# Kernel tuning notes

Hardware: AMD Instinct MI355X
Metric: run time of the kernel (lower is better)

The kernel has to match this reference:

```python
import jax, jax.numpy as jnp
import numpy as np

EPS = 1e-8
K_KNN = 20

def vn_lin(W, x):
    # W: [Cout, Cin], x: [B, Cin, 3, ...] -> [B, Cout, 3, ...]
    return jnp.einsum('oi,bi...->bo...', W, x)

def vn_relu(Wd, x):
    # VNLeakyReLU with negative_slope=0, share_nonlinearity=False
    d = jnp.einsum('oi,bi...->bo...', Wd, x)
    dot = jnp.sum(x * d, axis=2, keepdims=True)   # sum over 3-vector axis
    dsq = jnp.sum(d * d, axis=2, keepdims=True) + EPS
    return jnp.where(dot >= 0, x, x - (dot / dsq) * d)

def graph_feature_cross(p, k):
    # p: [B, N, 3] -> feat: [B, 3, 3, N, k]
    xx = jnp.sum(p * p, axis=-1)                       # [B,N]
    inner = jnp.einsum('bnd,bmd->bnm', p, p)           # [B,N,N]
    neg_dist = 2.0 * inner - xx[:, :, None] - xx[:, None, :]
    idx = jax.lax.top_k(neg_dist, k)[1]                # [B,N,k] nearest neighbors
    nbrs = jax.vmap(lambda pb, ib: pb[ib])(p, idx)     # [B,N,k,3]
    xr = jnp.broadcast_to(p[:, :, None, :], nbrs.shape)
    cross = jnp.cross(nbrs, xr)                        # [B,N,k,3]
    feat = jnp.stack([nbrs - xr, xr, cross], axis=3)   # [B,N,k,3(ch),3(vec)]
    return jnp.transpose(feat, (0, 3, 4, 1, 2))        # [B,3,3,N,k]

def setup_inputs() -> dict:
    key = jax.random.key(0)
    ks = jax.random.split(key, 9)
    B, N = 4, 2048
    H = 128           # hidden_dim // 3
    C_IN = 2 * H      # 256
    CC = 128          # c_dim // 3
    s_in = 1.0 / np.sqrt(C_IN)
    s_h = 1.0 / np.sqrt(H)
    return {
        'p': jax.random.normal(ks[0], (B, N, 3), dtype=jnp.float32),
        'fc_pos_W': jax.random.normal(ks[1], (C_IN, 3), dtype=jnp.float32) / np.sqrt(3.0),
        'blk_d0': jax.random.normal(ks[2], (5, C_IN, C_IN), dtype=jnp.float32) * s_in,
        'blk_W0': jax.random.normal(ks[3], (5, H, C_IN), dtype=jnp.float32) * s_in,
        'blk_d1': jax.random.normal(ks[4], (5, H, H), dtype=jnp.float32) * s_h,
        'blk_W1': jax.random.normal(ks[5], (5, H, H), dtype=jnp.float32) * s_h,
        'blk_Ws': jax.random.normal(ks[6], (5, H, C_IN), dtype=jnp.float32) * s_in,
        'fc_c_W': jax.random.normal(ks[7], (CC, H), dtype=jnp.float32) * s_h,
        'act_d': jax.random.normal(ks[8], (H, H), dtype=jnp.float32) * s_h,
    }

def reference(p, fc_pos_W, blk_d0, blk_W0, blk_d1, blk_W1, blk_Ws, fc_c_W, act_d):
    feat = graph_feature_cross(p, K_KNN)          # [B,3,3,N,k]
    x = vn_lin(fc_pos_W, feat)                    # [B,256,3,N,k]
    net = jnp.mean(x, axis=-1)                    # mean_pool over k -> [B,256,3,N]

    def block(i, x):
        h = vn_lin(blk_W0[i], vn_relu(blk_d0[i], x))
        dx = vn_lin(blk_W1[i], vn_relu(blk_d1[i], h))
        return vn_lin(blk_Ws[i], x) + dx          # shortcut (size_in != size_out)

    net = block(0, net)                           # [B,128,3,N]
    for i in range(1, 5):
        pooled = jnp.broadcast_to(jnp.mean(net, axis=3, keepdims=True), net.shape)
        net = block(i, jnp.concatenate([net, pooled], axis=1))
    net = jnp.mean(net, axis=3)                   # [B,128,3]
    c = vn_lin(fc_c_W, vn_relu(act_d, net))       # [B,128,3]
    return c.reshape(c.shape[0], -1)              # [B,384]
```

## Files before the change

kernel.cpp:

```cpp
#include <hip/hip_runtime.h>
#include <math.h>

#define N_PTS 2048
#define K_NN  20
#define K_D   10
#define WTOT  819200

typedef unsigned short u16;
typedef unsigned int   u32;
typedef _Float16 f16;
using half8   = __attribute__((ext_vector_type(8))) _Float16;
using floatx4 = __attribute__((ext_vector_type(4))) float;

__device__ __forceinline__ void split2h(float v, f16& h, f16& l) {
    h = (f16)v;
    l = (f16)((v - (float)h) * 1024.0f);
}

__device__ __forceinline__ float neg_dist(float4 q2, float4 c) {
    return fmaf(q2.x, c.x, fmaf(q2.y, c.y, fmaf(q2.z, c.z, -q2.w))) - c.w;
}

__global__ __launch_bounds__(256) void prep_kernel(
    const float* __restrict__ pts, float* __restrict__ m_out,
    const float* __restrict__ bd0, const float* __restrict__ bW0,
    const float* __restrict__ bd1, const float* __restrict__ bW1,
    const float* __restrict__ bWs, u16* __restrict__ Wswz,
    float* __restrict__ nm_acc)
{
    __shared__ float4 sp[N_PTS];
    if (blockIdx.x >= 1024) {
        int i = (blockIdx.x - 1024) * 256 + threadIdx.x;
        if (i >= WTOT) return;
        if (i < 7680) nm_acc[i] = 0.f;
        float v; int base, K, local;
        if (i < 327680)      { int rel = i;          base = (rel/65536)*65536;            local = rel%65536; K = 256; v = bd0[rel]; }
        else if (i < 491520) { int rel = i - 327680; base = 327680 + (rel/32768)*32768;   local = rel%32768; K = 256; v = bW0[rel]; }
        else if (i < 573440) { int rel = i - 491520; base = 491520 + (rel/16384)*16384;   local = rel%16384; K = 128; v = bd1[rel]; }
        else if (i < 655360) { int rel = i - 573440; base = 573440 + (rel/16384)*16384;   local = rel%16384; K = 128; v = bW1[rel]; }
        else                 { int rel = i - 655360; base = 655360 + (rel/32768)*32768;   local = rel%32768; K = 256; v = bWs[rel]; }
        int m = local / K, k = local % K;
        int NKF = K >> 5;
        int mf = m >> 4, r = m & 15;
        int kf = k >> 5, q = (k >> 3) & 3, ii = k & 7;
        int lane = q*16 + r;
        int dst = base + ((mf*NKF + kf)*64 + lane)*8 + ii;
        f16 h, l; split2h(v, h, l);
        f16* W = (f16*)Wswz;
        W[dst] = h; W[WTOT + dst] = l;
        return;
    }

    const int b     = blockIdx.x >> 8;
    const int qbase = (blockIdx.x & 255) << 3;
    const int ql    = threadIdx.x >> 5;
    const int sl    = threadIdx.x & 31;
    const float* pb = pts + (size_t)b * N_PTS * 3;
    for (int i = threadIdx.x; i < N_PTS; i += 256) {
        float x = pb[i*3+0], y = pb[i*3+1], z = pb[i*3+2];
        sp[i] = make_float4(x, y, z, x*x + y*y + z*z);
    }
    __syncthreads();

    const int n = qbase + ql;
    const float4 q = sp[n];
    const float4 q2 = make_float4(2.f*q.x, 2.f*q.y, 2.f*q.z, q.w);

    float t[K_D];
#pragma unroll
    for (int s = 0; s < K_D; ++s) t[s] = -INFINITY;

    for (int j = 0; j < N_PTS/32; ++j) {
        float4 c = sp[j*32 + sl];
        float v = neg_dist(q2, c);
#pragma unroll
        for (int s = 0; s < K_D; ++s) {
            float nx = (s < K_D-1) ? t[s+1] : INFINITY;
            t[s] = fminf(fmaxf(t[s], v), nx);
        }
    }

    float head = t[K_D-1];
    float T = -INFINITY;
#pragma unroll 1
    for (int e = 0; e < K_NN; ++e) {
        float v = head; int w = sl;
#pragma unroll
        for (int off = 1; off < 32; off <<= 1) {
            float vo = __shfl_xor(v, off);
            int   wo = __shfl_xor(w, off);
            bool take = (vo > v) || (vo == v && wo < w);
            v = take ? vo : v;
            w = take ? wo : w;
        }
        T = v;
        if (w == sl) {
#pragma unroll
            for (int s = K_D-1; s > 0; --s) t[s] = t[s-1];
            t[0] = -INFINITY;
            head = t[K_D-1];
        }
    }

    float sx = 0.f, sy = 0.f, sz = 0.f;
    for (int j = 0; j < N_PTS/32; ++j) {
        float4 c = sp[j*32 + sl];
        float v = neg_dist(q2, c);
        if (v >= T) { sx += c.x; sy += c.y; sz += c.z; }
    }
#pragma unroll
    for (int off = 1; off < 32; off <<= 1) {
        sx += __shfl_xor(sx, off);
        sy += __shfl_xor(sy, off);
        sz += __shfl_xor(sz, off);
    }
    if (sl == 0) {
        const float inv = 1.0f / (float)K_NN;
        const int pt = b * N_PTS + n;
        m_out[pt*3+0] = sx * inv;
        m_out[pt*3+1] = sy * inv;
        m_out[pt*3+2] = sz * inv;
    }
}

template<int MF, int JF>
__device__ __forceinline__ void run_gemm_hi(
    const f16* __restrict__ Whi, size_t aoff,
    int NK, const f16* Blds, int bstride, int lane,
    floatx4 (&acc)[MF][JF])
{
    const int l15 = lane & 15;
    const int lq8 = (lane >> 4) * 8;
    half8 Aa[MF], Ab[MF];

    auto loada = [&](half8 (&dst)[MF], int kf) {
#pragma unroll
        for (int fm = 0; fm < MF; ++fm)
            dst[fm] = *(const half8*)(Whi + aoff + (size_t)(fm*NK + kf)*512 + (size_t)lane*8);
    };
    auto step = [&](half8 (&af)[MF], int kf) {
        half8 bq[JF];
#pragma unroll
        for (int fj = 0; fj < JF; ++fj)
            bq[fj] = *(const half8*)&Blds[(fj*16 + l15)*bstride + kf*32 + lq8];
#pragma unroll
        for (int fm = 0; fm < MF; ++fm)
#pragma unroll
            for (int fj = 0; fj < JF; ++fj)
                acc[fm][fj] = __builtin_amdgcn_mfma_f32_16x16x32_f16(af[fm], bq[fj], acc[fm][fj], 0, 0, 0);
    };

    loada(Aa, 0);
#pragma unroll 1
    for (int kf = 0; kf < NK; kf += 2) {
        loada(Ab, kf + 1);
        step(Aa, kf);
        if (kf + 2 < NK) loada(Aa, kf + 2);
        step(Ab, kf + 1);
    }
}

template<int MF, int JF>
__device__ __forceinline__ void run_gemm_split(
    const f16* __restrict__ Whi, const f16* __restrict__ Wlo, size_t aoff,
    int NK, const f16* Blds, int bstride, int lane,
    floatx4 (&acc)[MF][JF], floatx4 (&accL)[MF][JF])
{
    const int l15 = lane & 15;
    const int lq8 = (lane >> 4) * 8;
    half8 Aa[2*MF], Ab[2*MF];

    auto loada = [&](half8 (&dst)[2*MF], int kf) {
#pragma unroll
        for (int fm = 0; fm < MF; ++fm) {
            size_t fo = aoff + (size_t)(fm*NK + kf)*512 + (size_t)lane*8;
            dst[fm*2+0] = *(const half8*)(Whi + fo);
            dst[fm*2+1] = *(const half8*)(Wlo + fo);
        }
    };
    auto step = [&](half8 (&af)[2*MF], int kf) {
        half8 bq[JF];
#pragma unroll
        for (int fj = 0; fj < JF; ++fj)
            bq[fj] = *(const half8*)&Blds[(fj*16 + l15)*bstride + kf*32 + lq8];
#pragma unroll
        for (int fm = 0; fm < MF; ++fm)
#pragma unroll
            for (int fj = 0; fj < JF; ++fj) {
                acc[fm][fj]  = __builtin_amdgcn_mfma_f32_16x16x32_f16(af[fm*2+0], bq[fj], acc[fm][fj], 0, 0, 0);
                accL[fm][fj] = __builtin_amdgcn_mfma_f32_16x16x32_f16(af[fm*2+1], bq[fj], accL[fm][fj], 0, 0, 0);
            }
    };

    loada(Aa, 0);
#pragma unroll 1
    for (int kf = 0; kf < NK; kf += 2) {
        loada(Ab, kf + 1);
        step(Aa, kf);
        if (kf + 2 < NK) loada(Aa, kf + 2);
        step(Ab, kf + 1);
    }
}

__device__ __forceinline__ uint2 pack_res(floatx4 a, floatx4 aL) {
    u16 hh[4];
#pragma unroll
    for (int r = 0; r < 4; ++r) {
        f16 hv = (f16)(a[r] + aL[r] * (1.0f/1024.0f));
        hh[r] = *(u16*)&hv;
    }
    uint2 pv;
    pv.x = (u32)hh[0] | ((u32)hh[1] << 16);
    pv.y = (u32)hh[2] | ((u32)hh[3] << 16);
    return pv;
}

__device__ __forceinline__ uint2 pack_hi(floatx4 a) {
    u16 hh[4];
#pragma unroll
    for (int r = 0; r < 4; ++r) {
        f16 hv = (f16)a[r];
        hh[r] = *(u16*)&hv;
    }
    uint2 pv;
    pv.x = (u32)hh[0] | ((u32)hh[1] << 16);
    pv.y = (u32)hh[2] | ((u32)hh[3] << 16);
    return pv;
}

__global__ __launch_bounds__(256, 3) void resblk_kernel(
    const u16* __restrict__ Wswz,
    int offD0, int offW0, int offD1, int offW1, int offWs,
    const f16* __restrict__ netIn, const float* __restrict__ nm_prev,
    const float* __restrict__ pts, const float* __restrict__ m_buf,
    const float* __restrict__ fcW,
    f16* __restrict__ netOut, float* __restrict__ nm_out, int blk0,
    int skip_store)
{
    __shared__ struct {
        f16 X[48*264];
        union { f16 d[48*264]; float C[48*132]; } Y;
    } s;

    const int tid  = threadIdx.x;
    const int jb   = blockIdx.x * 48;
    const int bB   = blockIdx.x >> 7;
    const int lane = tid & 63;
    const int wv   = tid >> 6;
    const f16* Whi = (const f16*)Wswz;
    const f16* Wlo = Whi + WTOT;

    if (blk0) {
        float* Hf = (float*)s.Y.C;
        const int ptbase = blockIdx.x * 16;
        for (int i = tid; i < 768; i += 256) Hf[i] = fcW[i];
        if (tid < 96) Hf[768 + tid] = (tid < 48) ? pts[ptbase*3 + tid]
                                                 : m_buf[ptbase*3 + tid - 48];
        __syncthreads();
#pragma unroll 1
        for (int it = 0; it < 6; ++it) {
            int idx = tid + 256*it;
            int r = idx >> 5;
            int cg = idx & 31;
            int l = r / 3, v = r - l*3;
            float pv0[3] = {Hf[768+l*3], Hf[768+l*3+1], Hf[768+l*3+2]};
            float mv0[3] = {Hf[816+l*3], Hf[816+l*3+1], Hf[816+l*3+2]};
            int v1 = (v==2) ? 0 : v+1;
            int v2 = (v==0) ? 2 : v-1;
            float av = mv0[v] - pv0[v];
            float bv = pv0[v];
            float cv = mv0[v1]*pv0[v2] - mv0[v2]*pv0[v1];
            half8 o;
#pragma unroll
            for (int k = 0; k < 8; ++k) {
                int ch = cg*8 + k;
                o[k] = (f16)(Hf[ch*3+0]*av + Hf[ch*3+1]*bv + Hf[ch*3+2]*cv);
            }
            *(half8*)&s.X[r*264 + cg*8] = o;
        }
    } else {
#pragma unroll 1
        for (int it = 0; it < 6; ++it) {
            int idx = tid + 256*it;
            int r = idx >> 5;
            int cg = idx & 31;
            if (cg < 16) {
                uint4 vv = *(const uint4*)(netIn + (size_t)(jb + r)*128 + cg*8);
                *(uint4*)&s.X[r*264 + cg*8] = vv;
            } else {
                int v = r % 3;
                const float* np = nm_prev + (bB*3+v)*128 + (cg-16)*8;
                half8 o;
#pragma unroll
                for (int k = 0; k < 8; ++k) o[k] = (f16)(np[k] * (1.0f/2048.0f));
                *(half8*)&s.X[r*264 + cg*8] = o;
            }
        }
    }
    __syncthreads();

    floatx4 acc4[2][3], accL4[2][3];
#pragma unroll
    for (int a = 0; a < 2; ++a)
#pragma unroll
        for (int b = 0; b < 3; ++b) { acc4[a][b] = (floatx4){0,0,0,0}; accL4[a][b] = (floatx4){0,0,0,0}; }

    {
        floatx4 acc[4][3];
#pragma unroll
        for (int a = 0; a < 4; ++a)
#pragma unroll
            for (int b = 0; b < 3; ++b) acc[a][b] = (floatx4){0,0,0,0};
        run_gemm_hi<4,3>(Whi, (size_t)offD0 + (size_t)wv*16384, 8, s.X, 264, lane, acc);
#pragma unroll
        for (int fm = 0; fm < 4; ++fm)
#pragma unroll
            for (int fj = 0; fj < 3; ++fj) {
                int mloc = wv*64 + fm*16 + (lane>>4)*4;
                int jl   = fj*16 + (lane & 15);
                *(uint2*)&s.Y.d[jl*264 + mloc] = pack_hi(acc[fm][fj]);
            }
    }
    __syncthreads();

    run_gemm_split<2,3>(Whi, Wlo, (size_t)offWs + (size_t)wv*8192, 8, s.X, 264, lane, acc4, accL4);

#pragma unroll 1
    for (int it = 0; it < 2; ++it) {
        int idx = tid + 256*it;
        int l = idx >> 5, cg = idx & 31;
        half8 xa = *(const half8*)&s.X[(l*3+0)*264 + cg*8];
        half8 xb = *(const half8*)&s.X[(l*3+1)*264 + cg*8];
        half8 xc = *(const half8*)&s.X[(l*3+2)*264 + cg*8];
        half8 da = *(const half8*)&s.Y.d[(l*3+0)*264 + cg*8];
        half8 db = *(const half8*)&s.Y.d[(l*3+1)*264 + cg*8];
        half8 dc = *(const half8*)&s.Y.d[(l*3+2)*264 + cg*8];
        half8 ya, yb, yc;
#pragma unroll
        for (int k = 0; k < 8; ++k) {
            float x0 = (float)xa[k], x1 = (float)xb[k], x2 = (float)xc[k];
            float d0 = (float)da[k], d1 = (float)db[k], d2 = (float)dc[k];
            float dot = x0*d0 + x1*d1 + x2*d2;
            float y0, y1, y2;
            if (dot >= 0.f) { y0 = x0; y1 = x1; y2 = x2; }
            else {
                float dsq = d0*d0 + d1*d1 + d2*d2 + 1e-8f;
                float sc = dot / dsq;
                y0 = x0 - sc*d0; y1 = x1 - sc*d1; y2 = x2 - sc*d2;
            }
            ya[k] = (f16)y0; yb[k] = (f16)y1; yc[k] = (f16)y2;
        }
        *(half8*)&s.Y.d[(l*3+0)*264 + cg*8] = ya;
        *(half8*)&s.Y.d[(l*3+1)*264 + cg*8] = yb;
        *(half8*)&s.Y.d[(l*3+2)*264 + cg*8] = yc;
    }
    __syncthreads();

    {
        floatx4 acc[2][3], accL[2][3];
#pragma unroll
        for (int a = 0; a < 2; ++a)
#pragma unroll
            for (int b = 0; b < 3; ++b) { acc[a][b] = (floatx4){0,0,0,0}; accL[a][b] = (floatx4){0,0,0,0}; }
        run_gemm_split<2,3>(Whi, Wlo, (size_t)offW0 + (size_t)wv*8192, 8, s.Y.d, 264, lane, acc, accL);
#pragma unroll
        for (int fm = 0; fm < 2; ++fm)
#pragma unroll
            for (int fj = 0; fj < 3; ++fj) {
                int mloc = wv*32 + fm*16 + (lane>>4)*4;
                int jl   = fj*16 + (lane & 15);
                *(uint2*)&s.X[jl*136 + mloc] = pack_res(acc[fm][fj], accL[fm][fj]);
            }
    }
    __syncthreads();

    {
        floatx4 acc[2][3];
#pragma unroll
        for (int a = 0; a < 2; ++a)
#pragma unroll
            for (int b = 0; b < 3; ++b) acc[a][b] = (floatx4){0,0,0,0};
        run_gemm_hi<2,3>(Whi, (size_t)offD1 + (size_t)wv*4096, 4, s.X, 136, lane, acc);
#pragma unroll
        for (int fm = 0; fm < 2; ++fm)
#pragma unroll
            for (int fj = 0; fj < 3; ++fj) {
                int mloc = wv*32 + fm*16 + (lane>>4)*4;
                int jl   = fj*16 + (lane & 15);
                *(uint2*)&s.Y.d[jl*136 + mloc] = pack_hi(acc[fm][fj]);
            }
    }
    __syncthreads();

    {
        int l = tid >> 4, cg = tid & 15;
        half8 xa = *(const half8*)&s.X[(l*3+0)*136 + cg*8];
        half8 xb = *(const half8*)&s.X[(l*3+1)*136 + cg*8];
        half8 xc = *(const half8*)&s.X[(l*3+2)*136 + cg*8];
        half8 da = *(const half8*)&s.Y.d[(l*3+0)*136 + cg*8];
        half8 db = *(const half8*)&s.Y.d[(l*3+1)*136 + cg*8];
        half8 dc = *(const half8*)&s.Y.d[(l*3+2)*136 + cg*8];
        half8 ya, yb, yc;
#pragma unroll
        for (int k = 0; k < 8; ++k) {
            float x0 = (float)xa[k], x1 = (float)xb[k], x2 = (float)xc[k];
            float d0 = (float)da[k], d1 = (float)db[k], d2 = (float)dc[k];
            float dot = x0*d0 + x1*d1 + x2*d2;
            float y0, y1, y2;
            if (dot >= 0.f) { y0 = x0; y1 = x1; y2 = x2; }
            else {
                float dsq = d0*d0 + d1*d1 + d2*d2 + 1e-8f;
                float sc = dot / dsq;
                y0 = x0 - sc*d0; y1 = x1 - sc*d1; y2 = x2 - sc*d2;
            }
            ya[k] = (f16)y0; yb[k] = (f16)y1; yc[k] = (f16)y2;
        }
        __syncthreads();
        *(half8*)&s.X[(l*3+0)*136 + cg*8] = ya;
        *(half8*)&s.X[(l*3+1)*136 + cg*8] = yb;
        *(half8*)&s.X[(l*3+2)*136 + cg*8] = yc;
    }
    __syncthreads();

    run_gemm_split<2,3>(Whi, Wlo, (size_t)offW1 + (size_t)wv*4096, 4, s.X, 136, lane, acc4, accL4);

#pragma unroll
    for (int fm = 0; fm < 2; ++fm)
#pragma unroll
        for (int fj = 0; fj < 3; ++fj) {
            int mloc = wv*32 + fm*16 + (lane>>4)*4;
            int jl   = fj*16 + (lane & 15);
            floatx4 res;
#pragma unroll
            for (int r = 0; r < 4; ++r) res[r] = acc4[fm][fj][r] + accL4[fm][fj][r] * (1.0f/1024.0f);
            if (!skip_store) {
                u16 hh[4];
#pragma unroll
                for (int r = 0; r < 4; ++r) { f16 hv = (f16)res[r]; hh[r] = *(u16*)&hv; }
                uint2 pv;
                pv.x = (u32)hh[0] | ((u32)hh[1] << 16);
                pv.y = (u32)hh[2] | ((u32)hh[3] << 16);
                *(uint2*)(netOut + (size_t)(jb + jl)*128 + mloc) = pv;
            }
            *(floatx4*)&s.Y.C[jl*132 + mloc] = res;
        }
    __syncthreads();

#pragma unroll 1
    for (int idx = tid; idx < 384; idx += 256) {
        int v = idx >> 7, ch = idx & 127;
        float sum = 0.f;
#pragma unroll 1
        for (int pt = 0; pt < 16; ++pt) sum += s.Y.C[(pt*3+v)*132 + ch];
        atomicAdd(nm_out + (bB*3+v)*128 + ch, sum);
    }
}

__global__ __launch_bounds__(128) void final_kernel(const float* __restrict__ nm_sum,
                                                    const float* __restrict__ act_d,
                                                    const float* __restrict__ fc_c,
                                                    float* __restrict__ out)
{
    const int b = blockIdx.x;
    const int c = threadIdx.x;
    __shared__ float xs[128][3];
    __shared__ float ys[128][3];
    xs[c][0] = nm_sum[(b*3+0)*128 + c] * (1.0f/2048.0f);
    xs[c][1] = nm_sum[(b*3+1)*128 + c] * (1.0f/2048.0f);
    xs[c][2] = nm_sum[(b*3+2)*128 + c] * (1.0f/2048.0f);
    __syncthreads();
    float d0 = 0.f, d1 = 0.f, d2 = 0.f;
    for (int i = 0; i < 128; ++i) {
        float w = act_d[c*128 + i];
        d0 = fmaf(w, xs[i][0], d0);
        d1 = fmaf(w, xs[i][1], d1);
        d2 = fmaf(w, xs[i][2], d2);
    }
    float x0 = xs[c][0], x1 = xs[c][1], x2 = xs[c][2];
    float dot = x0*d0 + x1*d1 + x2*d2;
    float y0, y1, y2;
    if (dot >= 0.f) { y0 = x0; y1 = x1; y2 = x2; }
    else {
        float dsq = d0*d0 + d1*d1 + d2*d2 + 1e-8f;
        float sc = dot / dsq;
        y0 = x0 - sc*d0; y1 = x1 - sc*d1; y2 = x2 - sc*d2;
    }
    ys[c][0] = y0; ys[c][1] = y1; ys[c][2] = y2;
    __syncthreads();
    float o0 = 0.f, o1 = 0.f, o2 = 0.f;
    for (int i = 0; i < 128; ++i) {
        float w = fc_c[c*128 + i];
        o0 = fmaf(w, ys[i][0], o0);
        o1 = fmaf(w, ys[i][1], o1);
        o2 = fmaf(w, ys[i][2], o2);
    }
    out[b*384 + c*3 + 0] = o0;
    out[b*384 + c*3 + 1] = o1;
    out[b*384 + c*3 + 2] = o2;
}

extern "C" void kernel_launch(void* const* d_in, const int* in_sizes, int n_in,
                              void* d_out, int out_size, void* d_ws, size_t ws_size,
                              hipStream_t stream)
{
    const float* p      = (const float*)d_in[0];
    const float* fc_pos = (const float*)d_in[1];
    const float* bd0    = (const float*)d_in[2];
    const float* bW0    = (const float*)d_in[3];
    const float* bd1    = (const float*)d_in[4];
    const float* bW1    = (const float*)d_in[5];
    const float* bWs    = (const float*)d_in[6];
    const float* fc_c   = (const float*)d_in[7];
    const float* act_d  = (const float*)d_in[8];
    float* out = (float*)d_out;

    char* w = (char*)d_ws;
    float* m_buf  = (float*)w;  w += 98304;
    float* nm_acc = (float*)w;  w += 5*1536*4;
    u16*   Wswz   = (u16*)w;    w += (size_t)2*WTOT*2;
    f16*   netA   = (f16*)w;    w += (size_t)24576*128*2;
    f16*   netB   = (f16*)w;    w += (size_t)24576*128*2;

    prep_kernel<<<dim3(1024 + 3200), dim3(256), 0, stream>>>(
        p, m_buf, bd0, bW0, bd1, bW1, bWs, Wswz, nm_acc);

    f16* nIn = netA;
    f16* nOut = netB;
    for (int blk = 0; blk < 5; ++blk) {
        const int offD0 = blk*65536;
        const int offW0 = 327680 + blk*32768;
        const int offD1 = 491520 + blk*16384;
        const int offW1 = 573440 + blk*16384;
        const int offWs = 655360 + blk*32768;
        const float* nmp = (blk == 0) ? nullptr : (nm_acc + (blk-1)*1536);
        resblk_kernel<<<dim3(512), dim3(256), 0, stream>>>(
            Wswz, offD0, offW0, offD1, offW1, offWs,
            (blk == 0) ? netA : nIn, nmp, p, m_buf, fc_pos,
            nOut, nm_acc + blk*1536, (blk == 0) ? 1 : 0,
            (blk == 4) ? 1 : 0);
        f16* tmp = nIn; nIn = nOut; nOut = tmp;
    }

    final_kernel<<<dim3(4), dim3(128), 0, stream>>>(nm_acc + 4*1536, act_d, fc_c, out);

    (void)in_sizes; (void)n_in; (void)out_size; (void)ws_size;
}
```

Measured before the change: 241.2 us.

## Fuse five residual blocks and final head into one persistent kernel with grid barrier

Replaces the five resblk launches and the final kernel with a single persistent kernel. Blocks loop over the residual stages, keep each block's point features resident in shared memory, and synchronize the global pooled means with an atomic-counter grid barrier. This removes launch overhead and the global fp16 round trip of the intermediate net tensor. It relies on all 512 blocks being co-resident (3 per CU is assumed), which risks deadlock otherwise, and adds barrier spin latency.

```diff
diff --git a/kernel.cpp b/kernel.cpp
--- a/kernel.cpp
+++ b/kernel.cpp
@@ -26,13 +26,14 @@
     const float* __restrict__ bd0, const float* __restrict__ bW0,
     const float* __restrict__ bd1, const float* __restrict__ bW1,
     const float* __restrict__ bWs, u16* __restrict__ Wswz,
-    float* __restrict__ nm_acc)
+    float* __restrict__ nm_acc, int* __restrict__ bar)
 {
     __shared__ float4 sp[N_PTS];
     if (blockIdx.x >= 1024) {
         int i = (blockIdx.x - 1024) * 256 + threadIdx.x;
         if (i >= WTOT) return;
         if (i < 7680) nm_acc[i] = 0.f;
+        if (i == 0) bar[0] = 0;
         float v; int base, K, local;
         if (i < 327680)      { int rel = i;          base = (rel/65536)*65536;            local = rel%65536; K = 256; v = bd0[rel]; }
         else if (i < 491520) { int rel = i - 327680; base = 327680 + (rel/32768)*32768;   local = rel%32768; K = 256; v = bW0[rel]; }
@@ -228,14 +229,25 @@
     return pv;
 }
 
-__global__ __launch_bounds__(256, 3) void resblk_kernel(
+__device__ __forceinline__ void grid_barrier(int* cnt, int target, int wait) {
+    __threadfence();
+    __syncthreads();
+    if (threadIdx.x == 0) {
+        atomicAdd(cnt, 1);
+        if (wait) {
+            while (atomicAdd(cnt, 0) < target) __builtin_amdgcn_s_sleep(16);
+        }
+    }
+    __syncthreads();
+}
+
+__global__ __launch_bounds__(256, 3) void mega_kernel(
     const u16* __restrict__ Wswz,
-    int offD0, int offW0, int offD1, int offW1, int offWs,
-    const f16* __restrict__ netIn, const float* __restrict__ nm_prev,
+    float* __restrict__ nm_acc, int* __restrict__ bar,
     const float* __restrict__ pts, const float* __restrict__ m_buf,
     const float* __restrict__ fcW,
-    f16* __restrict__ netOut, float* __restrict__ nm_out, int blk0,
-    int skip_store)
+    const float* __restrict__ act_d, const float* __restrict__ fc_c,
+    float* __restrict__ out)
 {
     __shared__ struct {
         f16 X[48*264];
@@ -243,103 +255,243 @@
     } s;
 
     const int tid  = threadIdx.x;
-    const int jb   = blockIdx.x * 48;
     const int bB   = blockIdx.x >> 7;
     const int lane = tid & 63;
     const int wv   = tid >> 6;
     const f16* Whi = (const f16*)Wswz;
     const f16* Wlo = Whi + WTOT;
 
-    if (blk0) {
-        float* Hf = (float*)s.Y.C;
-        const int ptbase = blockIdx.x * 16;
-        for (int i = tid; i < 768; i += 256) Hf[i] = fcW[i];
-        if (tid < 96) Hf[768 + tid] = (tid < 48) ? pts[ptbase*3 + tid]
-                                                 : m_buf[ptbase*3 + tid - 48];
-        __syncthreads();
-#pragma unroll 1
-        for (int it = 0; it < 6; ++it) {
+#pragma unroll 1
+    for (int blk = 0; blk < 5; ++blk) {
+        const int offD0 = blk*65536;
+        const int offW0 = 327680 + blk*32768;
+        const int offD1 = 491520 + blk*16384;
+        const int offW1 = 573440 + blk*16384;
+        const int offWs = 655360 + blk*32768;
+        float* nm_out = nm_acc + blk*1536;
+
+        if (blk == 0) {
+            float* Hf = (float*)s.Y.C;
+            const int ptbase = blockIdx.x * 16;
+            for (int i = tid; i < 768; i += 256) Hf[i] = fcW[i];
+            if (tid < 96) Hf[768 + tid] = (tid < 48) ? pts[ptbase*3 + tid]
+                                                     : m_buf[ptbase*3 + tid - 48];
+            __syncthreads();
+#pragma unroll 1
+            for (int it = 0; it < 6; ++it) {
+                int idx = tid + 256*it;
+                int r = idx >> 5;
+                int cgp = idx & 31;
+                int l = r / 3, v = r - l*3;
+                float pv0[3] = {Hf[768+l*3], Hf[768+l*3+1], Hf[768+l*3+2]};
+                float mv0[3] = {Hf[816+l*3], Hf[816+l*3+1], Hf[816+l*3+2]};
+                int v1 = (v==2) ? 0 : v+1;
+                int v2 = (v==0) ? 2 : v-1;
+                float av = mv0[v] - pv0[v];
+                float bv = pv0[v];
+                float cv = mv0[v1]*pv0[v2] - mv0[v2]*pv0[v1];
+                half8 o;
+#pragma unroll
+                for (int k = 0; k < 8; ++k) {
+                    int ch = cgp*8 + k;
+                    o[k] = (f16)(Hf[ch*3+0]*av + Hf[ch*3+1]*bv + Hf[ch*3+2]*cv);
+                }
+                *(half8*)&s.X[r*264 + cgp*8] = o;
+            }
+        } else {
+            f16* nmv = &s.Y.d[0];
+#pragma unroll 1
+            for (int idx = tid; idx < 384; idx += 256) {
+                int v = idx >> 7, ch = idx & 127;
+                float sv = atomicAdd(&nm_acc[(blk-1)*1536 + (bB*3+v)*128 + ch], 0.0f);
+                nmv[v*128 + ch] = (f16)(sv * (1.0f/2048.0f));
+            }
+            __syncthreads();
+#pragma unroll 1
+            for (int it = 0; it < 3; ++it) {
+                int idx = tid + 256*it;
+                int r = idx >> 4;
+                int cgp = idx & 15;
+                int v = r % 3;
+                *(uint4*)&s.X[r*264 + 128 + cgp*8] = *(const uint4*)&nmv[v*128 + cgp*8];
+            }
+        }
+        __syncthreads();
+
+        floatx4 acc4[2][3], accL4[2][3];
+#pragma unroll
+        for (int a = 0; a < 2; ++a)
+#pragma unroll
+            for (int b = 0; b < 3; ++b) { acc4[a][b] = (floatx4){0,0,0,0}; accL4[a][b] = (floatx4){0,0,0,0}; }
+
+        {
+            floatx4 acc[4][3];
+#pragma unroll
+            for (int a = 0; a < 4; ++a)
+#pragma unroll
+                for (int b = 0; b < 3; ++b) acc[a][b] = (floatx4){0,0,0,0};
+            run_gemm_hi<4,3>(Whi, (size_t)offD0 + (size_t)wv*16384, 8, s.X, 264, lane, acc);
+#pragma unroll
+            for (int fm = 0; fm < 4; ++fm)
+#pragma unroll
+                for (int fj = 0; fj < 3; ++fj) {
+                    int mloc = wv*64 + fm*16 + (lane>>4)*4;
+                    int jl   = fj*16 + (lane & 15);
+                    *(uint2*)&s.Y.d[jl*264 + mloc] = pack_hi(acc[fm][fj]);
+                }
+        }
+        __syncthreads();
+
+        run_gemm_split<2,3>(Whi, Wlo, (size_t)offWs + (size_t)wv*8192, 8, s.X, 264, lane, acc4, accL4);
+
+#pragma unroll 1
+        for (int it = 0; it < 2; ++it) {
             int idx = tid + 256*it;
-            int r = idx >> 5;
-            int cg = idx & 31;
-            int l = r / 3, v = r - l*3;
-            float pv0[3] = {Hf[768+l*3], Hf[768+l*3+1], Hf[768+l*3+2]};
-            float mv0[3] = {Hf[816+l*3], Hf[816+l*3+1], Hf[816+l*3+2]};
-            int v1 = (v==2) ? 0 : v+1;
-            int v2 = (v==0) ? 2 : v-1;
-            float av = mv0[v] - pv0[v];
-            float bv = pv0[v];
-            float cv = mv0[v1]*pv0[v2] - mv0[v2]*pv0[v1];
-            half8 o;
+            int l = idx >> 5, cgp = idx & 31;
+            half8 xa = *(const half8*)&s.X[(l*3+0)*264 + cgp*8];
+            half8 xb = *(const half8*)&s.X[(l*3+1)*264 + cgp*8];
+            half8 xc = *(const half8*)&s.X[(l*3+2)*264 + cgp*8];
+            half8 da = *(const half8*)&s.Y.d[(l*3+0)*264 + cgp*8];
+            half8 db = *(const half8*)&s.Y.d[(l*3+1)*264 + cgp*8];
+            half8 dc = *(const half8*)&s.Y.d[(l*3+2)*264 + cgp*8];
+            half8 ya, yb, yc;
 #pragma unroll
             for (int k = 0; k < 8; ++k) {
-                int ch = cg*8 + k;
-                o[k] = (f16)(Hf[ch*3+0]*av + Hf[ch*3+1]*bv + Hf[ch*3+2]*cv);
-            }
-            *(half8*)&s.X[r*264 + cg*8] = o;
-        }
-    } else {
-#pragma unroll 1
-        for (int it = 0; it < 6; ++it) {
-            int idx = tid + 256*it;
-            int r = idx >> 5;
-            int cg = idx & 31;
-            if (cg < 16) {
-                uint4 vv = *(const uint4*)(netIn + (size_t)(jb + r)*128 + cg*8);
-                *(uint4*)&s.X[r*264 + cg*8] = vv;
-            } else {
-                int v = r % 3;
-                const float* np = nm_prev + (bB*3+v)*128 + (cg-16)*8;
-                half8 o;
-#pragma unroll
-                for (int k = 0; k < 8; ++k) o[k] = (f16)(np[k] * (1.0f/2048.0f));
-                *(half8*)&s.X[r*264 + cg*8] = o;
-            }
-        }
-    }
-    __syncthreads();
-
-    floatx4 acc4[2][3], accL4[2][3];
-#pragma unroll
-    for (int a = 0; a < 2; ++a)
-#pragma unroll
-        for (int b = 0; b < 3; ++b) { acc4[a][b] = (floatx4){0,0,0,0}; accL4[a][b] = (floatx4){0,0,0,0}; }
-
-    {
-        floatx4 acc[4][3];
-#pragma unroll
-        for (int a = 0; a < 4; ++a)
-#pragma unroll
-            for (int b = 0; b < 3; ++b) acc[a][b] = (floatx4){0,0,0,0};
-        run_gemm_hi<4,3>(Whi, (size_t)offD0 + (size_t)wv*16384, 8, s.X, 264, lane, acc);
-#pragma unroll
-        for (int fm = 0; fm < 4; ++fm)
+                float x0 = (float)xa[k], x1 = (float)xb[k], x2 = (float)xc[k];
+                float d0 = (float)da[k], d1 = (float)db[k], d2 = (float)dc[k];
+                float dot = x0*d0 + x1*d1 + x2*d2;
+                float y0, y1, y2;
+                if (dot >= 0.f) { y0 = x0; y1 = x1; y2 = x2; }
+                else {
+                    float dsq = d0*d0 + d1*d1 + d2*d2 + 1e-8f;
+                    float sc = dot / dsq;
+                    y0 = x0 - sc*d0; y1 = x1 - sc*d1; y2 = x2 - sc*d2;
+                }
+                ya[k] = (f16)y0; yb[k] = (f16)y1; yc[k] = (f16)y2;
+            }
+            *(half8*)&s.Y.d[(l*3+0)*264 + cgp*8] = ya;
+            *(half8*)&s.Y.d[(l*3+1)*264 + cgp*8] = yb;
+            *(half8*)&s.Y.d[(l*3+2)*264 + cgp*8] = yc;
+        }
+        __syncthreads();
+
+        {
+            floatx4 acc[2][3], accL[2][3];
+#pragma unroll
+            for (int a = 0; a < 2; ++a)
+#pragma unroll
+                for (int b = 0; b < 3; ++b) { acc[a][b] = (floatx4){0,0,0,0}; accL[a][b] = (floatx4){0,0,0,0}; }
+            run_gemm_split<2,3>(Whi, Wlo, (size_t)offW0 + (size_t)wv*8192, 8, s.Y.d, 264, lane, acc, accL);
+#pragma unroll
+            for (int fm = 0; fm < 2; ++fm)
+#pragma unroll
+                for (int fj = 0; fj < 3; ++fj) {
+                    int mloc = wv*32 + fm*16 + (lane>>4)*4;
+                    int jl   = fj*16 + (lane & 15);
+                    *(uint2*)&s.X[jl*136 + mloc] = pack_res(acc[fm][fj], accL[fm][fj]);
+                }
+        }
+        __syncthreads();
+
+        {
+            floatx4 acc[2][3];
+#pragma unroll
+            for (int a = 0; a < 2; ++a)
+#pragma unroll
+                for (int b = 0; b < 3; ++b) acc[a][b] = (floatx4){0,0,0,0};
+            run_gemm_hi<2,3>(Whi, (size_t)offD1 + (size_t)wv*4096, 4, s.X, 136, lane, acc);
+#pragma unroll
+            for (int fm = 0; fm < 2; ++fm)
+#pragma unroll
+                for (int fj = 0; fj < 3; ++fj) {
+                    int mloc = wv*32 + fm*16 + (lane>>4)*4;
+                    int jl   = fj*16 + (lane & 15);
+                    *(uint2*)&s.Y.d[jl*136 + mloc] = pack_hi(acc[fm][fj]);
+                }
+        }
+        __syncthreads();
+
+        {
+            int l = tid >> 4, cgp = tid & 15;
+            half8 xa = *(const half8*)&s.X[(l*3+0)*136 + cgp*8];
+            half8 xb = *(const half8*)&s.X[(l*3+1)*136 + cgp*8];
+            half8 xc = *(const half8*)&s.X[(l*3+2)*136 + cgp*8];
+            half8 da = *(const half8*)&s.Y.d[(l*3+0)*136 + cgp*8];
+            half8 db = *(const half8*)&s.Y.d[(l*3+1)*136 + cgp*8];
+            half8 dc = *(const half8*)&s.Y.d[(l*3+2)*136 + cgp*8];
+            half8 ya, yb, yc;
+#pragma unroll
+            for (int k = 0; k < 8; ++k) {
+                float x0 = (float)xa[k], x1 = (float)xb[k], x2 = (float)xc[k];
+                float d0 = (float)da[k], d1 = (float)db[k], d2 = (float)dc[k];
+                float dot = x0*d0 + x1*d1 + x2*d2;
+                float y0, y1, y2;
+                if (dot >= 0.f) { y0 = x0; y1 = x1; y2 = x2; }
+                else {
+                    float dsq = d0*d0 + d1*d1 + d2*d2 + 1e-8f;
+                    float sc = dot / dsq;
+                    y0 = x0 - sc*d0; y1 = x1 - sc*d1; y2 = x2 - sc*d2;
+                }
+                ya[k] = (f16)y0; yb[k] = (f16)y1; yc[k] = (f16)y2;
+            }
+            __syncthreads();
+            *(half8*)&s.X[(l*3+0)*136 + cgp*8] = ya;
+            *(half8*)&s.X[(l*3+1)*136 + cgp*8] = yb;
+            *(half8*)&s.X[(l*3+2)*136 + cgp*8] = yc;
+        }
+        __syncthreads();
+
+        run_gemm_split<2,3>(Whi, Wlo, (size_t)offW1 + (size_t)wv*4096, 4, s.X, 136, lane, acc4, accL4);
+        __syncthreads();
+
+#pragma unroll
+        for (int fm = 0; fm < 2; ++fm)
 #pragma unroll
             for (int fj = 0; fj < 3; ++fj) {
-                int mloc = wv*64 + fm*16 + (lane>>4)*4;
+                int mloc = wv*32 + fm*16 + (lane>>4)*4;
                 int jl   = fj*16 + (lane & 15);
-                *(uint2*)&s.Y.d[jl*264 + mloc] = pack_hi(acc[fm][fj]);
-            }
-    }
-    __syncthreads();
-
-    run_gemm_split<2,3>(Whi, Wlo, (size_t)offWs + (size_t)wv*8192, 8, s.X, 264, lane, acc4, accL4);
-
-#pragma unroll 1
-    for (int it = 0; it < 2; ++it) {
-        int idx = tid + 256*it;
-        int l = idx >> 5, cg = idx & 31;
-        half8 xa = *(const half8*)&s.X[(l*3+0)*264 + cg*8];
-        half8 xb = *(const half8*)&s.X[(l*3+1)*264 + cg*8];
-        half8 xc = *(const half8*)&s.X[(l*3+2)*264 + cg*8];
-        half8 da = *(const half8*)&s.Y.d[(l*3+0)*264 + cg*8];
-        half8 db = *(const half8*)&s.Y.d[(l*3+1)*264 + cg*8];
-        half8 dc = *(const half8*)&s.Y.d[(l*3+2)*264 + cg*8];
-        half8 ya, yb, yc;
-#pragma unroll
-        for (int k = 0; k < 8; ++k) {
-            float x0 = (float)xa[k], x1 = (float)xb[k], x2 = (float)xc[k];
-            float d0 = (float)da[k], d1 = (float)db[k], d2 = (float)dc[k];
+                floatx4 res;
+#pragma unroll
+                for (int r = 0; r < 4; ++r) res[r] = acc4[fm][fj][r] + accL4[fm][fj][r] * (1.0f/1024.0f);
+                *(uint2*)&s.X[jl*264 + mloc] = pack_res(acc4[fm][fj], accL4[fm][fj]);
+                *(floatx4*)&s.Y.C[jl*132 + mloc] = res;
+            }
+        __syncthreads();
+
+#pragma unroll 1
+        for (int idx = tid; idx < 384; idx += 256) {
+            int v = idx >> 7, ch = idx & 127;
+            float sum = 0.f;
+#pragma unroll 1
+            for (int pt = 0; pt < 16; ++pt) sum += s.Y.C[(pt*3+v)*132 + ch];
+            atomicAdd(nm_out + (bB*3+v)*128 + ch, sum);
+        }
+
+        int need_wait = (blk < 4) || (blockIdx.x < 4);
+        grid_barrier(bar, 512*(blk+1), need_wait);
+    }
+
+    if (blockIdx.x < 4) {
+        const int b = blockIdx.x;
+        float* xs = s.Y.C;
+        float* ys = s.Y.C + 384;
+        float* nm4 = nm_acc + 4*1536;
+        const int c = tid & 127;
+        if (tid < 128) {
+            xs[c*3+0] = atomicAdd(&nm4[(b*3+0)*128 + c], 0.0f) * (1.0f/2048.0f);
+            xs[c*3+1] = atomicAdd(&nm4[(b*3+1)*128 + c], 0.0f) * (1.0f/2048.0f);
+            xs[c*3+2] = atomicAdd(&nm4[(b*3+2)*128 + c], 0.0f) * (1.0f/2048.0f);
+        }
+        __syncthreads();
+        if (tid < 128) {
+            float d0 = 0.f, d1 = 0.f, d2 = 0.f;
+            for (int i = 0; i < 128; ++i) {
+                float w = act_d[c*128 + i];
+                d0 = fmaf(w, xs[i*3+0], d0);
+                d1 = fmaf(w, xs[i*3+1], d1);
+                d2 = fmaf(w, xs[i*3+2], d2);
+            }
+            float x0 = xs[c*3+0], x1 = xs[c*3+1], x2 = xs[c*3+2];
             float dot = x0*d0 + x1*d1 + x2*d2;
             float y0, y1, y2;
             if (dot >= 0.f) { y0 = x0; y1 = x1; y2 = x2; }
@@ -348,155 +500,22 @@
                 float sc = dot / dsq;
                 y0 = x0 - sc*d0; y1 = x1 - sc*d1; y2 = x2 - sc*d2;
             }
-            ya[k] = (f16)y0; yb[k] = (f16)y1; yc[k] = (f16)y2;
-        }
-        *(half8*)&s.Y.d[(l*3+0)*264 + cg*8] = ya;
-        *(half8*)&s.Y.d[(l*3+1)*264 + cg*8] = yb;
-        *(half8*)&s.Y.d[(l*3+2)*264 + cg*8] = yc;
-    }
-    __syncthreads();
-
-    {
-        floatx4 acc[2][3], accL[2][3];
-#pragma unroll
-        for (int a = 0; a < 2; ++a)
-#pragma unroll
-            for (int b = 0; b < 3; ++b) { acc[a][b] = (floatx4){0,0,0,0}; accL[a][b] = (floatx4){0,0,0,0}; }
-        run_gemm_split<2,3>(Whi, Wlo, (size_t)offW0 + (size_t)wv*8192, 8, s.Y.d, 264, lane, acc, accL);
-#pragma unroll
-        for (int fm = 0; fm < 2; ++fm)
-#pragma unroll
-            for (int fj = 0; fj < 3; ++fj) {
-                int mloc = wv*32 + fm*16 + (lane>>4)*4;
-                int jl   = fj*16 + (lane & 15);
-                *(uint2*)&s.X[jl*136 + mloc] = pack_res(acc[fm][fj], accL[fm][fj]);
-            }
-    }
-    __syncthreads();
-
-    {
-        floatx4 acc[2][3];
-#pragma unroll
-        for (int a = 0; a < 2; ++a)
-#pragma unroll
-            for (int b = 0; b < 3; ++b) acc[a][b] = (floatx4){0,0,0,0};
-        run_gemm_hi<2,3>(Whi, (size_t)offD1 + (size_t)wv*4096, 4, s.X, 136, lane, acc);
-#pragma unroll
-        for (int fm = 0; fm < 2; ++fm)
-#pragma unroll
-            for (int fj = 0; fj < 3; ++fj) {
-                int mloc = wv*32 + fm*16 + (lane>>4)*4;
-                int jl   = fj*16 + (lane & 15);
-                *(uint2*)&s.Y.d[jl*136 + mloc] = pack_hi(acc[fm][fj]);
-            }
-    }
-    __syncthreads();
-
-    {
-        int l = tid >> 4, cg = tid & 15;
-        half8 xa = *(const half8*)&s.X[(l*3+0)*136 + cg*8];
-        half8 xb = *(const half8*)&s.X[(l*3+1)*136 + cg*8];
-        half8 xc = *(const half8*)&s.X[(l*3+2)*136 + cg*8];
-        half8 da = *(const half8*)&s.Y.d[(l*3+0)*136 + cg*8];
-        half8 db = *(const half8*)&s.Y.d[(l*3+1)*136 + cg*8];
-        half8 dc = *(const half8*)&s.Y.d[(l*3+2)*136 + cg*8];
-        half8 ya, yb, yc;
-#pragma unroll
-        for (int k = 0; k < 8; ++k) {
-            float x0 = (float)xa[k], x1 = (float)xb[k], x2 = (float)xc[k];
-            float d0 = (float)da[k], d1 = (float)db[k], d2 = (float)dc[k];
-            float dot = x0*d0 + x1*d1 + x2*d2;
-            float y0, y1, y2;
-            if (dot >= 0.f) { y0 = x0; y1 = x1; y2 = x2; }
-            else {
-                float dsq = d0*d0 + d1*d1 + d2*d2 + 1e-8f;
-                float sc = dot / dsq;
-                y0 = x0 - sc*d0; y1 = x1 - sc*d1; y2 = x2 - sc*d2;
-            }
-            ya[k] = (f16)y0; yb[k] = (f16)y1; yc[k] = (f16)y2;
-        }
-        __syncthreads();
-        *(half8*)&s.X[(l*3+0)*136 + cg*8] = ya;
-        *(half8*)&s.X[(l*3+1)*136 + cg*8] = yb;
-        *(half8*)&s.X[(l*3+2)*136 + cg*8] = yc;
-    }
-    __syncthreads();
-
-    run_gemm_split<2,3>(Whi, Wlo, (size_t)offW1 + (size_t)wv*4096, 4, s.X, 136, lane, acc4, accL4);
-
-#pragma unroll
-    for (int fm = 0; fm < 2; ++fm)
-#pragma unroll
-        for (int fj = 0; fj < 3; ++fj) {
-            int mloc = wv*32 + fm*16 + (lane>>4)*4;
-            int jl   = fj*16 + (lane & 15);
-            floatx4 res;
-#pragma unroll
-            for (int r = 0; r < 4; ++r) res[r] = acc4[fm][fj][r] + accL4[fm][fj][r] * (1.0f/1024.0f);
-            if (!skip_store) {
-                u16 hh[4];
-#pragma unroll
-                for (int r = 0; r < 4; ++r) { f16 hv = (f16)res[r]; hh[r] = *(u16*)&hv; }
-                uint2 pv;
-                pv.x = (u32)hh[0] | ((u32)hh[1] << 16);
-                pv.y = (u32)hh[2] | ((u32)hh[3] << 16);
-                *(uint2*)(netOut + (size_t)(jb + jl)*128 + mloc) = pv;
-            }
-            *(floatx4*)&s.Y.C[jl*132 + mloc] = res;
-        }
-    __syncthreads();
-
-#pragma unroll 1
-    for (int idx = tid; idx < 384; idx += 256) {
-        int v = idx >> 7, ch = idx & 127;
-        float sum = 0.f;
-#pragma unroll 1
-        for (int pt = 0; pt < 16; ++pt) sum += s.Y.C[(pt*3+v)*132 + ch];
-        atomicAdd(nm_out + (bB*3+v)*128 + ch, sum);
-    }
-}
-
-__global__ __launch_bounds__(128) void final_kernel(const float* __restrict__ nm_sum,
-                                                    const float* __restrict__ act_d,
-                                                    const float* __restrict__ fc_c,
-                                                    float* __restrict__ out)
-{
-    const int b = blockIdx.x;
-    const int c = threadIdx.x;
-    __shared__ float xs[128][3];
-    __shared__ float ys[128][3];
-    xs[c][0] = nm_sum[(b*3+0)*128 + c] * (1.0f/2048.0f);
-    xs[c][1] = nm_sum[(b*3+1)*128 + c] * (1.0f/2048.0f);
-    xs[c][2] = nm_sum[(b*3+2)*128 + c] * (1.0f/2048.0f);
-    __syncthreads();
-    float d0 = 0.f, d1 = 0.f, d2 = 0.f;
-    for (int i = 0; i < 128; ++i) {
-        float w = act_d[c*128 + i];
-        d0 = fmaf(w, xs[i][0], d0);
-        d1 = fmaf(w, xs[i][1], d1);
-        d2 = fmaf(w, xs[i][2], d2);
-    }
-    float x0 = xs[c][0], x1 = xs[c][1], x2 = xs[c][2];
-    float dot = x0*d0 + x1*d1 + x2*d2;
-    float y0, y1, y2;
-    if (dot >= 0.f) { y0 = x0; y1 = x1; y2 = x2; }
-    else {
-        float dsq = d0*d0 + d1*d1 + d2*d2 + 1e-8f;
-        float sc = dot / dsq;
-        y0 = x0 - sc*d0; y1 = x1 - sc*d1; y2 = x2 - sc*d2;
-    }
-    ys[c][0] = y0; ys[c][1] = y1; ys[c][2] = y2;
-    __syncthreads();
-    float o0 = 0.f, o1 = 0.f, o2 = 0.f;
-    for (int i = 0; i < 128; ++i) {
-        float w = fc_c[c*128 + i];
-        o0 = fmaf(w, ys[i][0], o0);
-        o1 = fmaf(w, ys[i][1], o1);
-        o2 = fmaf(w, ys[i][2], o2);
-    }
-    out[b*384 + c*3 + 0] = o0;
-    out[b*384 + c*3 + 1] = o1;
-    out[b*384 + c*3 + 2] = o2;
+            ys[c*3+0] = y0; ys[c*3+1] = y1; ys[c*3+2] = y2;
+        }
+        __syncthreads();
+        if (tid < 128) {
+            float o0 = 0.f, o1 = 0.f, o2 = 0.f;
+            for (int i = 0; i < 128; ++i) {
+                float w = fc_c[c*128 + i];
+                o0 = fmaf(w, ys[i*3+0], o0);
+                o1 = fmaf(w, ys[i*3+1], o1);
+                o2 = fmaf(w, ys[i*3+2], o2);
+            }
+            out[b*384 + c*3 + 0] = o0;
+            out[b*384 + c*3 + 1] = o1;
+            out[b*384 + c*3 + 2] = o2;
+        }
+    }
 }
 
 extern "C" void kernel_launch(void* const* d_in, const int* in_sizes, int n_in,
@@ -517,31 +536,14 @@
     char* w = (char*)d_ws;
     float* m_buf  = (float*)w;  w += 98304;
     float* nm_acc = (float*)w;  w += 5*1536*4;
+    int*   bar    = (int*)w;    w += 16;
     u16*   Wswz   = (u16*)w;    w += (size_t)2*WTOT*2;
-    f16*   netA   = (f16*)w;    w += (size_t)24576*128*2;
-    f16*   netB   = (f16*)w;    w += (size_t)24576*128*2;
 
     prep_kernel<<<dim3(1024 + 3200), dim3(256), 0, stream>>>(
-        p, m_buf, bd0, bW0, bd1, bW1, bWs, Wswz, nm_acc);
-
-    f16* nIn = netA;
-    f16* nOut = netB;
-    for (int blk = 0; blk < 5; ++blk) {
-        const int offD0 = blk*65536;
-        const int offW0 = 327680 + blk*32768;
-        const int offD1 = 491520 + blk*16384;
-        const int offW1 = 573440 + blk*16384;
-        const int offWs = 655360 + blk*32768;
-        const float* nmp = (blk == 0) ? nullptr : (nm_acc + (blk-1)*1536);
-        resblk_kernel<<<dim3(512), dim3(256), 0, stream>>>(
-            Wswz, offD0, offW0, offD1, offW1, offWs,
-            (blk == 0) ? netA : nIn, nmp, p, m_buf, fc_pos,
-            nOut, nm_acc + blk*1536, (blk == 0) ? 1 : 0,
-            (blk == 4) ? 1 : 0);
-        f16* tmp = nIn; nIn = nOut; nOut = tmp;
-    }
-
-    final_kernel<<<dim3(4), dim3(128), 0, stream>>>(nm_acc + 4*1536, act_d, fc_c, out);
+        p, m_buf, bd0, bW0, bd1, bW1, bWs, Wswz, nm_acc, bar);
+
+    mega_kernel<<<dim3(512), dim3(256), 0, stream>>>(
+        Wswz, nm_acc, bar, p, m_buf, fc_pos, act_d, fc_c, out);
 
     (void)in_sizes; (void)n_in; (void)out_size; (void)ws_size;
 }
```

Result: slower. 476.0 us (+97.3%).
